# Performance work log

Hardware: AMD Instinct MI355X
Metric: run time of the kernel (lower is better)

## Reference

```python
import jax, jax.numpy as jnp
import numpy as np

BN_EPS = 1e-5


def setup_inputs() -> dict:
    key = jax.random.key(0)
    k1, k2, k3 = jax.random.split(key, 3)
    n, d = 4096, 128
    x = jax.random.normal(k1, (2 * n, d), dtype=jnp.float32)
    affinity_A = jax.random.normal(k2, (n, n), dtype=jnp.float32)
    # Xavier-uniform-like init for the [d, d] weight
    lim = float(np.sqrt(6.0 / (d + d)))
    weight = jax.random.uniform(k3, (d, d), dtype=jnp.float32, minval=-lim, maxval=lim)
    gamma = jnp.ones((d,), dtype=jnp.float32)
    beta = jnp.zeros((d,), dtype=jnp.float32)
    return {"x": x, "affinity_A": affinity_A, "weight": weight, "gamma": gamma, "beta": beta}


def reference(x, affinity_A, weight, gamma, beta):
    # Binarize affinity
    A = jnp.where(affinity_A > 0, 1.0, 0.0).astype(x.dtype)  # [n, n]
    n = A.shape[0]
    I = jnp.eye(n, dtype=x.dtype)
    # Block adjacency [[A, I], [I, A]] -> [2n, 2n]
    adj = jnp.block([[A, I], [I, A]])
    # Symmetric normalization D^{-1/2} A D^{-1/2}.
    # (Original code materializes D^{-1/2} as a full matrix and does two O(n^3)
    # matmuls; mathematically it is just row/column scaling, done here directly.)
    deg = adj.sum(axis=1)                 # [2n], >= 1 because of identity blocks
    dinv = deg ** -0.5
    norm_A = dinv[:, None] * adj * dinv[None, :]
    # GCN propagation: (norm_A @ x) @ W
    h = (norm_A @ x) @ weight             # [2n, d]
    # BatchNorm1d (training mode, biased variance) + ReLU
    mean = h.mean(axis=0)
    var = h.var(axis=0)
    h = (h - mean) * jax.lax.rsqrt(var + BN_EPS) * gamma + beta
    return jax.nn.relu(h)
```

## Files before the change

### kernel.cpp

```cpp
#include <hip/hip_runtime.h>
#include <stdint.h>


#define N_NODES 4096
#define D 128
#define TWO_N (2*N_NODES)
#define SK 8
#define KCH (N_NODES / SK)

typedef unsigned short u16;
typedef __bf16 bf16;
typedef bf16 bf16x8 __attribute__((ext_vector_type(8)));
typedef float f32x4 __attribute__((ext_vector_type(4)));
typedef u16 u16x8 __attribute__((ext_vector_type(8)));

__device__ __forceinline__ float bf2f(u16 u) {
    return __builtin_bit_cast(float, ((unsigned)u) << 16);
}
__device__ __forceinline__ u16 f2bf(float f) {
    unsigned b = __builtin_bit_cast(unsigned, f);
    unsigned r = (b + 0x7FFFu + ((b >> 16) & 1u)) >> 16;
    return (u16)r;
}
__device__ __forceinline__ bool det_fp32(const u16* gamma) {
    return gamma[0] != (u16)0x3F80;
}

__global__ void k_deg(const void* __restrict__ aff, const u16* __restrict__ gamma,
                      float* __restrict__ dinv, uint32_t* __restrict__ pack32) {
    int t = threadIdx.x;
    bool fp32 = det_fp32(gamma);
    int rl = t >> 7;
    int row = blockIdx.x * 2 + rl;
    int cl = t & 127;
    unsigned bits = 0;
    if (!fp32) {
        const u16* p = (const u16*)aff + (size_t)row * N_NODES + cl * 32;
        u16x8 v0 = *reinterpret_cast<const u16x8*>(p);
        u16x8 v1 = *reinterpret_cast<const u16x8*>(p + 8);
        u16x8 v2 = *reinterpret_cast<const u16x8*>(p + 16);
        u16x8 v3 = *reinterpret_cast<const u16x8*>(p + 24);
        #pragma unroll
        for (int e = 0; e < 8; ++e) {
            bits |= (((short)v0[e] > 0) ? 1u : 0u) << e;
            bits |= (((short)v1[e] > 0) ? 1u : 0u) << (8 + e);
            bits |= (((short)v2[e] > 0) ? 1u : 0u) << (16 + e);
            bits |= (((short)v3[e] > 0) ? 1u : 0u) << (24 + e);
        }
    } else {
        const float* p = (const float*)aff + (size_t)row * N_NODES + cl * 32;
        #pragma unroll
        for (int q = 0; q < 8; ++q) {
            f32x4 v = *reinterpret_cast<const f32x4*>(p + q * 4);
            #pragma unroll
            for (int e = 0; e < 4; ++e)
                bits |= ((v[e] > 0.f) ? 1u : 0u) << (q * 4 + e);
        }
    }
    pack32[(size_t)row * 128 + cl] = bits;
    int cnt = __popc(bits);
    #pragma unroll
    for (int off = 32; off; off >>= 1) cnt += __shfl_down(cnt, off, 64);
    __shared__ int sc[4];
    if ((t & 63) == 0) sc[t >> 6] = cnt;
    __syncthreads();
    if (t < 2)
        dinv[blockIdx.x * 2 + t] = rsqrtf((float)(sc[t * 2] + sc[t * 2 + 1] + 1));
}

__global__ void k_scale(const void* __restrict__ x, const void* __restrict__ W,
                        const u16* __restrict__ gamma, const float* __restrict__ dinv,
                        u16* __restrict__ XsT, u16* __restrict__ WT) {
    int t = threadIdx.x;
    bool fp32 = det_fp32(gamma);

    if (blockIdx.x >= 512) {
        const u16* W16 = (const u16*)W;
        const float* W32 = (const float*)W;
        int o = (blockIdx.x - 512) * 16 + (t >> 4);
        int cg = (t & 15) * 8;
        u16x8 wv;
        #pragma unroll
        for (int e = 0; e < 8; ++e) {
            size_t wi = (size_t)(cg + e) * D + o;
            float v = fp32 ? W32[wi] : bf2f(W16[wi]);
            wv[e] = f2bf(v);
        }
        *reinterpret_cast<u16x8*>(WT + (size_t)o * D + cg) = wv;
        return;
    }

    __shared__ u16 sx[16 * 136];
    int j0 = blockIdx.x * 8;
    {
        int rr = t >> 4;
        int c0 = (t & 15) * 8;
        size_t grow = (rr < 8) ? (size_t)(j0 + rr) : (size_t)(N_NODES + j0 + rr - 8);
        float dv = dinv[j0 + (rr & 7)];
        u16x8 o;
        if (!fp32) {
            u16x8 xv = *reinterpret_cast<const u16x8*>((const u16*)x + grow * D + c0);
            #pragma unroll
            for (int e = 0; e < 8; ++e) o[e] = f2bf(dv * bf2f(xv[e]));
        } else {
            f32x4 xa = *reinterpret_cast<const f32x4*>((const float*)x + grow * D + c0);
            f32x4 xb = *reinterpret_cast<const f32x4*>((const float*)x + grow * D + c0 + 4);
            #pragma unroll
            for (int e = 0; e < 4; ++e) {
                o[e] = f2bf(dv * xa[e]);
                o[4 + e] = f2bf(dv * xb[e]);
            }
        }
        *reinterpret_cast<u16x8*>(sx + rr * 136 + c0) = o;
    }
    __syncthreads();
    {
        int c = t;
        int rbase = (c < 128) ? 0 : 8;
        int cl = c & 127;
        u16x8 o;
        #pragma unroll
        for (int jl = 0; jl < 8; ++jl) o[jl] = sx[(rbase + jl) * 136 + cl];
        *reinterpret_cast<u16x8*>(XsT + (size_t)c * N_NODES + j0) = o;
    }
}

__launch_bounds__(256)
__global__ void k_gemm(const uint32_t* __restrict__ pack32, const u16* __restrict__ XsT,
                       u16* __restrict__ Ypart) {
    int t = threadIdx.x;
    int mt = blockIdx.x >> 3;
    int sk = blockIdx.x & 7;
    int r0 = mt * 64;
    int k0 = sk * KCH;
    int lane = t & 63, wid = t >> 6;
    int quad = lane >> 4, l15 = lane & 15;
    int shift = quad * 8;

    f32x4 acc[4][4];
    #pragma unroll
    for (int i = 0; i < 4; ++i)
        #pragma unroll
        for (int j = 0; j < 4; ++j) acc[i][j] = (f32x4){0.f, 0.f, 0.f, 0.f};

    const u16* bp[4];
    #pragma unroll
    for (int j = 0; j < 4; ++j)
        bp[j] = XsT + (size_t)(wid * 64 + j * 16 + l15) * N_NODES + k0 + quad * 8;
    const uint32_t* ap[4];
    #pragma unroll
    for (int i = 0; i < 4; ++i)
        ap[i] = pack32 + (size_t)(r0 + i * 16 + l15) * 128 + (k0 >> 5);

    u16x8 bc[2][4][2];
    uint2 ac[2][4];

    #pragma unroll
    for (int j = 0; j < 4; ++j)
        #pragma unroll
        for (int ks = 0; ks < 2; ++ks)
            bc[0][j][ks] = *reinterpret_cast<const u16x8*>(bp[j] + ks * 32);
    #pragma unroll
    for (int i = 0; i < 4; ++i) ac[0][i] = *reinterpret_cast<const uint2*>(ap[i]);

    #pragma unroll
    for (int it = 0; it < KCH / 64; ++it) {
        int cur = it & 1, nxt = cur ^ 1;
        if (it < KCH / 64 - 1) {
            int off = (it + 1) * 64;
            #pragma unroll
            for (int j = 0; j < 4; ++j)
                #pragma unroll
                for (int ks = 0; ks < 2; ++ks)
                    bc[nxt][j][ks] = *reinterpret_cast<const u16x8*>(bp[j] + off + ks * 32);
            #pragma unroll
            for (int i = 0; i < 4; ++i)
                ac[nxt][i] = *reinterpret_cast<const uint2*>(ap[i] + (it + 1) * 2);
        }
        #pragma unroll
        for (int ks = 0; ks < 2; ++ks) {
            bf16x8 af[4];
            #pragma unroll
            for (int i = 0; i < 4; ++i) {
                unsigned d = ks ? ac[cur][i].y : ac[cur][i].x;
                unsigned by = (d >> shift) & 0xFFu;
                u16x8 e;
                #pragma unroll
                for (int e2 = 0; e2 < 8; ++e2)
                    e[e2] = ((by >> e2) & 1u) ? (u16)0x3F80 : (u16)0;
                af[i] = __builtin_bit_cast(bf16x8, e);
            }
            #pragma unroll
            for (int i = 0; i < 4; ++i)
                #pragma unroll
                for (int j = 0; j < 4; ++j)
                    acc[i][j] = __builtin_amdgcn_mfma_f32_16x16x32_bf16(
                        af[i], __builtin_bit_cast(bf16x8, bc[cur][j][ks]), acc[i][j], 0, 0, 0);
        }
    }

    u16* yp = Ypart + (size_t)sk * N_NODES * 256;
    #pragma unroll
    for (int i = 0; i < 4; ++i) {
        int row = r0 + i * 16 + quad * 4;
        #pragma unroll
        for (int j = 0; j < 4; ++j) {
            int col = wid * 64 + j * 16 + l15;
            #pragma unroll
            for (int r = 0; r < 4; ++r)
                yp[(size_t)(row + r) * 256 + col] = f2bf(acc[i][j][r]);
        }
    }
}

__global__ void k_comb(const u16* __restrict__ Ypart, const void* __restrict__ x,
                       const u16* __restrict__ WT, const u16* __restrict__ gamma,
                       const float* __restrict__ dinv, u16* __restrict__ hpre,
                       float* __restrict__ pS, float* __restrict__ pQ) {
    __shared__ u16 sH[16 * 136];
    __shared__ u16 sWT[128 * 136];
    __shared__ float sOut[16 * 132];
    int t = threadIdx.x;
    bool fp32 = det_fp32(gamma);
    int r0 = blockIdx.x * 16;
    bool top = blockIdx.x < 256;
    int node0 = top ? r0 : r0 - N_NODES;
    const u16* x16 = (const u16*)x;
    const float* x32 = (const float*)x;

    {
        int r = t >> 4;
        int c0 = (t & 15) * 8;
        int node = node0 + r;
        int ycol = (top ? 0 : 128) + c0;
        float fs[8] = {0.f, 0.f, 0.f, 0.f, 0.f, 0.f, 0.f, 0.f};
        #pragma unroll
        for (int sk = 0; sk < SK; ++sk) {
            u16x8 yv = *reinterpret_cast<const u16x8*>(Ypart + ((size_t)sk * N_NODES + node) * 256 + ycol);
            #pragma unroll
            for (int e = 0; e < 8; ++e) fs[e] += bf2f(yv[e]);
        }
        float dv = dinv[node];
        size_t xi = (top ? (size_t)(N_NODES + node) : (size_t)node) * D + c0;
        u16x8 hv;
        if (!fp32) {
            u16x8 xv = *reinterpret_cast<const u16x8*>(x16 + xi);
            #pragma unroll
            for (int e = 0; e < 8; ++e) hv[e] = f2bf(dv * fs[e] + dv * dv * bf2f(xv[e]));
        } else {
            f32x4 xa = *reinterpret_cast<const f32x4*>(x32 + xi);
            f32x4 xb = *reinterpret_cast<const f32x4*>(x32 + xi + 4);
            #pragma unroll
            for (int e = 0; e < 4; ++e) {
                hv[e]     = f2bf(dv * fs[e]     + dv * dv * xa[e]);
                hv[4 + e] = f2bf(dv * fs[4 + e] + dv * dv * xb[e]);
            }
        }
        *reinterpret_cast<u16x8*>(sH + r * 136 + c0) = hv;
    }
    #pragma unroll
    for (int p = 0; p < 8; ++p) {
        int idx = p * 256 + t;
        int o = idx >> 4;
        int cg = (idx & 15) * 8;
        u16x8 wv = *reinterpret_cast<const u16x8*>(WT + (size_t)o * D + cg);
        *reinterpret_cast<u16x8*>(sWT + o * 136 + cg) = wv;
    }
    __syncthreads();

    int lane = t & 63, wid = t >> 6;
    int quad = lane >> 4, l15 = lane & 15;
    f32x4 acc[2];
    acc[0] = (f32x4){0.f, 0.f, 0.f, 0.f};
    acc[1] = (f32x4){0.f, 0.f, 0.f, 0.f};
    #pragma unroll
    for (int ks = 0; ks < 4; ++ks) {
        bf16x8 af = *reinterpret_cast<const bf16x8*>(sH + l15 * 136 + ks * 32 + quad * 8);
        #pragma unroll
        for (int j = 0; j < 2; ++j) {
            bf16x8 bfr = *reinterpret_cast<const bf16x8*>(sWT + (wid * 32 + j * 16 + l15) * 136 + ks * 32 + quad * 8);
            acc[j] = __builtin_amdgcn_mfma_f32_16x16x32_bf16(af, bfr, acc[j], 0, 0, 0);
        }
    }
    #pragma unroll
    for (int j = 0; j < 2; ++j) {
        int row = quad * 4;
        int col = wid * 32 + j * 16 + l15;
        #pragma unroll
        for (int r = 0; r < 4; ++r) sOut[(row + r) * 132 + col] = acc[j][r];
    }
    __syncthreads();
    #pragma unroll
    for (int p = 0; p < 8; ++p) {
        int idx = p * 256 + t;
        int r = idx >> 7, c = idx & 127;
        hpre[(size_t)(r0 + r) * D + c] = f2bf(sOut[r * 132 + c]);
    }
    if (t < 128) {
        float s = 0.f, q = 0.f;
        #pragma unroll
        for (int r = 0; r < 16; ++r) {
            float v = sOut[r * 132 + t];
            s += v; q += v * v;
        }
        pS[blockIdx.x * 128 + t] = s;
        pQ[blockIdx.x * 128 + t] = q;
    }
}

__global__ void k_stats(const float* __restrict__ pS, const float* __restrict__ pQ,
                        const void* __restrict__ gamma, const void* __restrict__ beta,
                        const u16* __restrict__ gdet, float* __restrict__ scsh) {
    __shared__ float rs[256], rq[256];
    int t = threadIdx.x;
    int c0 = blockIdx.x * 8;
    int cl = t & 7;
    int rr = t >> 3;
    float s = 0.f, q = 0.f;
    #pragma unroll
    for (int i = 0; i < 16; ++i) {
        int row = rr + i * 32;
        s += pS[row * 128 + c0 + cl];
        q += pQ[row * 128 + c0 + cl];
    }
    rs[t] = s; rq[t] = q;
    __syncthreads();
    #pragma unroll
    for (int st = 128; st >= 8; st >>= 1) {
        if (t < st) { rs[t] += rs[t + st]; rq[t] += rq[t + st]; }
        __syncthreads();
    }
    if (t < 8) {
        bool fp32 = det_fp32(gdet);
        int c = c0 + t;
        float mean = rs[t] * (1.0f / TWO_N);
        float var = fmaxf(rq[t] * (1.0f / TWO_N) - mean * mean, 0.f);
        float inv = rsqrtf(var + 1e-5f);
        float g = fp32 ? ((const float*)gamma)[c] : bf2f(((const u16*)gamma)[c]);
        float b = fp32 ? ((const float*)beta)[c]  : bf2f(((const u16*)beta)[c]);
        scsh[c] = inv * g;
        scsh[128 + c] = b - mean * inv * g;
    }
}

__global__ void k_bn(const u16* __restrict__ hpre, const float* __restrict__ scsh,
                     const u16* __restrict__ gdet, void* __restrict__ out) {
    __shared__ float ssc[128], ssh[128];
    int t = threadIdx.x;
    bool fp32 = det_fp32(gdet);
    if (t < 128) { ssc[t] = scsh[t]; ssh[t] = scsh[128 + t]; }
    __syncthreads();
    size_t base = (size_t)blockIdx.x * 2048 + t * 8;
    int c0 = (t & 15) * 8;
    u16x8 hv = *reinterpret_cast<const u16x8*>(hpre + base);
    if (!fp32) {
        u16x8 ov;
        #pragma unroll
        for (int e = 0; e < 8; ++e) {
            float v = bf2f(hv[e]) * ssc[c0 + e] + ssh[c0 + e];
            ov[e] = f2bf(fmaxf(v, 0.f));
        }
        *reinterpret_cast<u16x8*>((u16*)out + base) = ov;
    } else {
        float* o = (float*)out + base;
        #pragma unroll
        for (int e = 0; e < 8; ++e) {
            float v = bf2f(hv[e]) * ssc[c0 + e] + ssh[c0 + e];
            o[e] = fmaxf(v, 0.f);
        }
    }
}

extern "C" void kernel_launch(void* const* d_in, const int* in_sizes, int n_in,
                              void* d_out, int out_size, void* d_ws, size_t ws_size,
                              hipStream_t stream) {
    const void* x = d_in[0];
    const void* aff = d_in[1];
    const void* W = d_in[2];
    const u16* gamma = (const u16*)d_in[3];
    const void* beta = d_in[4];

    char* ws = (char*)d_ws;
    uint32_t* pack32 = (uint32_t*)ws;
    u16* XsT = (u16*)(ws + 2097152);
    u16* Ypart = (u16*)(ws + 4194304);
    u16* hpre = (u16*)(ws + 20971520);
    float* dinv = (float*)(ws + 23068672);
    u16* WT = (u16*)(ws + 23085056);
    float* pS = (float*)(ws + 23117824);
    float* pQ = (float*)(ws + 23379968);
    float* scsh = (float*)(ws + 23642112);

    k_deg<<<2048, 256, 0, stream>>>(aff, gamma, dinv, pack32);
    k_scale<<<520, 256, 0, stream>>>(x, W, gamma, dinv, XsT, WT);
    k_gemm<<<512, 256, 0, stream>>>(pack32, XsT, Ypart);
    k_comb<<<512, 256, 0, stream>>>(Ypart, x, WT, gamma, dinv, hpre, pS, pQ);
    k_stats<<<16, 256, 0, stream>>>(pS, pQ, gamma, beta, gamma, scsh);
    k_bn<<<512, 256, 0, stream>>>(hpre, scsh, gamma, d_out);
}
```

Before: 145.3 us.

## Shrink gemm row tile to 32, triple-buffer loads, widen comb tile to 32 rows

The binarized-adjacency GEMM now uses 32-row tiles instead of 64, doubling the grid to 1024 blocks with a launch-bounds occupancy hint. The K loop steps 32 at a time with a three-stage register prefetch ring. The combine kernel now processes 32 rows per block with a 2x2 warp layout, halving its grid and the partial-stat rows that k_stats must reduce. The aim is more parallelism and latency hiding in the main GEMM at the cost of re-reading the XsT operand twice as often.

```diff
diff --git a/kernel.cpp b/kernel.cpp
--- a/kernel.cpp
+++ b/kernel.cpp
@@ -125,21 +125,21 @@
     }
 }
 
-__launch_bounds__(256)
+__launch_bounds__(256, 4)
 __global__ void k_gemm(const uint32_t* __restrict__ pack32, const u16* __restrict__ XsT,
                        u16* __restrict__ Ypart) {
     int t = threadIdx.x;
     int mt = blockIdx.x >> 3;
     int sk = blockIdx.x & 7;
-    int r0 = mt * 64;
+    int r0 = mt * 32;
     int k0 = sk * KCH;
     int lane = t & 63, wid = t >> 6;
     int quad = lane >> 4, l15 = lane & 15;
     int shift = quad * 8;
 
-    f32x4 acc[4][4];
-    #pragma unroll
-    for (int i = 0; i < 4; ++i)
+    f32x4 acc[2][4];
+    #pragma unroll
+    for (int i = 0; i < 2; ++i)
         #pragma unroll
         for (int j = 0; j < 4; ++j) acc[i][j] = (f32x4){0.f, 0.f, 0.f, 0.f};
 
@@ -147,61 +147,52 @@
     #pragma unroll
     for (int j = 0; j < 4; ++j)
         bp[j] = XsT + (size_t)(wid * 64 + j * 16 + l15) * N_NODES + k0 + quad * 8;
-    const uint32_t* ap[4];
-    #pragma unroll
-    for (int i = 0; i < 4; ++i)
+    const uint32_t* ap[2];
+    #pragma unroll
+    for (int i = 0; i < 2; ++i)
         ap[i] = pack32 + (size_t)(r0 + i * 16 + l15) * 128 + (k0 >> 5);
 
-    u16x8 bc[2][4][2];
-    uint2 ac[2][4];
-
-    #pragma unroll
-    for (int j = 0; j < 4; ++j)
-        #pragma unroll
-        for (int ks = 0; ks < 2; ++ks)
-            bc[0][j][ks] = *reinterpret_cast<const u16x8*>(bp[j] + ks * 32);
-    #pragma unroll
-    for (int i = 0; i < 4; ++i) ac[0][i] = *reinterpret_cast<const uint2*>(ap[i]);
-
-    #pragma unroll
-    for (int it = 0; it < KCH / 64; ++it) {
-        int cur = it & 1, nxt = cur ^ 1;
-        if (it < KCH / 64 - 1) {
-            int off = (it + 1) * 64;
+    u16x8 bb[3][4];
+    uint32_t ab[3][2];
+    #pragma unroll
+    for (int s = 0; s < 2; ++s) {
+        #pragma unroll
+        for (int j = 0; j < 4; ++j) bb[s][j] = *reinterpret_cast<const u16x8*>(bp[j] + s * 32);
+        #pragma unroll
+        for (int i = 0; i < 2; ++i) ab[s][i] = ap[i][s];
+    }
+
+    #pragma unroll
+    for (int s = 0; s < KCH / 32; ++s) {
+        int cur = s % 3, pre = (s + 2) % 3;
+        if (s < KCH / 32 - 2) {
             #pragma unroll
             for (int j = 0; j < 4; ++j)
-                #pragma unroll
-                for (int ks = 0; ks < 2; ++ks)
-                    bc[nxt][j][ks] = *reinterpret_cast<const u16x8*>(bp[j] + off + ks * 32);
-            #pragma unroll
-            for (int i = 0; i < 4; ++i)
-                ac[nxt][i] = *reinterpret_cast<const uint2*>(ap[i] + (it + 1) * 2);
-        }
-        #pragma unroll
-        for (int ks = 0; ks < 2; ++ks) {
-            bf16x8 af[4];
-            #pragma unroll
-            for (int i = 0; i < 4; ++i) {
-                unsigned d = ks ? ac[cur][i].y : ac[cur][i].x;
-                unsigned by = (d >> shift) & 0xFFu;
-                u16x8 e;
-                #pragma unroll
-                for (int e2 = 0; e2 < 8; ++e2)
-                    e[e2] = ((by >> e2) & 1u) ? (u16)0x3F80 : (u16)0;
-                af[i] = __builtin_bit_cast(bf16x8, e);
-            }
-            #pragma unroll
-            for (int i = 0; i < 4; ++i)
-                #pragma unroll
-                for (int j = 0; j < 4; ++j)
-                    acc[i][j] = __builtin_amdgcn_mfma_f32_16x16x32_bf16(
-                        af[i], __builtin_bit_cast(bf16x8, bc[cur][j][ks]), acc[i][j], 0, 0, 0);
-        }
+                bb[pre][j] = *reinterpret_cast<const u16x8*>(bp[j] + (s + 2) * 32);
+            #pragma unroll
+            for (int i = 0; i < 2; ++i) ab[pre][i] = ap[i][s + 2];
+        }
+        bf16x8 af[2];
+        #pragma unroll
+        for (int i = 0; i < 2; ++i) {
+            unsigned by = (ab[cur][i] >> shift) & 0xFFu;
+            u16x8 e;
+            #pragma unroll
+            for (int e2 = 0; e2 < 8; ++e2)
+                e[e2] = ((by >> e2) & 1u) ? (u16)0x3F80 : (u16)0;
+            af[i] = __builtin_bit_cast(bf16x8, e);
+        }
+        #pragma unroll
+        for (int i = 0; i < 2; ++i)
+            #pragma unroll
+            for (int j = 0; j < 4; ++j)
+                acc[i][j] = __builtin_amdgcn_mfma_f32_16x16x32_bf16(
+                    af[i], __builtin_bit_cast(bf16x8, bb[cur][j]), acc[i][j], 0, 0, 0);
     }
 
     u16* yp = Ypart + (size_t)sk * N_NODES * 256;
     #pragma unroll
-    for (int i = 0; i < 4; ++i) {
+    for (int i = 0; i < 2; ++i) {
         int row = r0 + i * 16 + quad * 4;
         #pragma unroll
         for (int j = 0; j < 4; ++j) {
@@ -217,19 +208,20 @@
                        const u16* __restrict__ WT, const u16* __restrict__ gamma,
                        const float* __restrict__ dinv, u16* __restrict__ hpre,
                        float* __restrict__ pS, float* __restrict__ pQ) {
-    __shared__ u16 sH[16 * 136];
+    __shared__ u16 sH[32 * 136];
     __shared__ u16 sWT[128 * 136];
-    __shared__ float sOut[16 * 132];
+    __shared__ float sOut[32 * 132];
     int t = threadIdx.x;
     bool fp32 = det_fp32(gamma);
-    int r0 = blockIdx.x * 16;
-    bool top = blockIdx.x < 256;
+    int r0 = blockIdx.x * 32;
+    bool top = blockIdx.x < 128;
     int node0 = top ? r0 : r0 - N_NODES;
     const u16* x16 = (const u16*)x;
     const float* x32 = (const float*)x;
 
-    {
-        int r = t >> 4;
+    #pragma unroll
+    for (int p = 0; p < 2; ++p) {
+        int r = p * 16 + (t >> 4);
         int c0 = (t & 15) * 8;
         int node = node0 + r;
         int ycol = (top ? 0 : 128) + c0;
@@ -269,29 +261,30 @@
     __syncthreads();
 
     int lane = t & 63, wid = t >> 6;
+    int wm2 = wid >> 1, wn2 = wid & 1;
     int quad = lane >> 4, l15 = lane & 15;
-    f32x4 acc[2];
-    acc[0] = (f32x4){0.f, 0.f, 0.f, 0.f};
-    acc[1] = (f32x4){0.f, 0.f, 0.f, 0.f};
+    f32x4 acc2[4];
+    #pragma unroll
+    for (int j = 0; j < 4; ++j) acc2[j] = (f32x4){0.f, 0.f, 0.f, 0.f};
     #pragma unroll
     for (int ks = 0; ks < 4; ++ks) {
-        bf16x8 af = *reinterpret_cast<const bf16x8*>(sH + l15 * 136 + ks * 32 + quad * 8);
-        #pragma unroll
-        for (int j = 0; j < 2; ++j) {
-            bf16x8 bfr = *reinterpret_cast<const bf16x8*>(sWT + (wid * 32 + j * 16 + l15) * 136 + ks * 32 + quad * 8);
-            acc[j] = __builtin_amdgcn_mfma_f32_16x16x32_bf16(af, bfr, acc[j], 0, 0, 0);
-        }
-    }
-    #pragma unroll
-    for (int j = 0; j < 2; ++j) {
-        int row = quad * 4;
-        int col = wid * 32 + j * 16 + l15;
-        #pragma unroll
-        for (int r = 0; r < 4; ++r) sOut[(row + r) * 132 + col] = acc[j][r];
-    }
-    __syncthreads();
-    #pragma unroll
-    for (int p = 0; p < 8; ++p) {
+        bf16x8 af = *reinterpret_cast<const bf16x8*>(sH + (wm2 * 16 + l15) * 136 + ks * 32 + quad * 8);
+        #pragma unroll
+        for (int j = 0; j < 4; ++j) {
+            bf16x8 bfr = *reinterpret_cast<const bf16x8*>(sWT + (wn2 * 64 + j * 16 + l15) * 136 + ks * 32 + quad * 8);
+            acc2[j] = __builtin_amdgcn_mfma_f32_16x16x32_bf16(af, bfr, acc2[j], 0, 0, 0);
+        }
+    }
+    #pragma unroll
+    for (int j = 0; j < 4; ++j) {
+        int row = wm2 * 16 + quad * 4;
+        int col = wn2 * 64 + j * 16 + l15;
+        #pragma unroll
+        for (int r = 0; r < 4; ++r) sOut[(row + r) * 132 + col] = acc2[j][r];
+    }
+    __syncthreads();
+    #pragma unroll
+    for (int p = 0; p < 16; ++p) {
         int idx = p * 256 + t;
         int r = idx >> 7, c = idx & 127;
         hpre[(size_t)(r0 + r) * D + c] = f2bf(sOut[r * 132 + c]);
@@ -299,7 +292,7 @@
     if (t < 128) {
         float s = 0.f, q = 0.f;
         #pragma unroll
-        for (int r = 0; r < 16; ++r) {
+        for (int r = 0; r < 32; ++r) {
             float v = sOut[r * 132 + t];
             s += v; q += v * v;
         }
@@ -318,7 +311,7 @@
     int rr = t >> 3;
     float s = 0.f, q = 0.f;
     #pragma unroll
-    for (int i = 0; i < 16; ++i) {
+    for (int i = 0; i < 8; ++i) {
         int row = rr + i * 32;
         s += pS[row * 128 + c0 + cl];
         q += pQ[row * 128 + c0 + cl];
@@ -388,13 +381,13 @@
     float* dinv = (float*)(ws + 23068672);
     u16* WT = (u16*)(ws + 23085056);
     float* pS = (float*)(ws + 23117824);
-    float* pQ = (float*)(ws + 23379968);
-    float* scsh = (float*)(ws + 23642112);
+    float* pQ = (float*)(ws + 23248896);
+    float* scsh = (float*)(ws + 23379968);
 
     k_deg<<<2048, 256, 0, stream>>>(aff, gamma, dinv, pack32);
     k_scale<<<520, 256, 0, stream>>>(x, W, gamma, dinv, XsT, WT);
-    k_gemm<<<512, 256, 0, stream>>>(pack32, XsT, Ypart);
-    k_comb<<<512, 256, 0, stream>>>(Ypart, x, WT, gamma, dinv, hpre, pS, pQ);
+    k_gemm<<<1024, 256, 0, stream>>>(pack32, XsT, Ypart);
+    k_comb<<<256, 256, 0, stream>>>(Ypart, x, WT, gamma, dinv, hpre, pS, pQ);
     k_stats<<<16, 256, 0, stream>>>(pS, pQ, gamma, beta, gamma, scsh);
     k_bn<<<512, 256, 0, stream>>>(hpre, scsh, gamma, d_out);
 }
```

New measurement: 157.1 us. 1.08x slower.

## Halve GEMM split-K, split output columns, enlarge combine tiles, move W transpose

Applied to the files above, without the earlier changes.

The main GEMM now splits K four ways instead of eight and instead splits the 256 output columns into two halves per block. This halves the bf16 partial-sum traffic that the combine kernel has to read and reduce. The combine kernel now processes 32 rows per block with a 2x2 wave layout, which halves the number of times the W tile is staged into shared memory. The W transpose moves from k_scale into extra blocks of k_deg, and the workspace offsets shrink to match. In exchange, each GEMM block re-reads the packed A bits for both column halves, and each block runs a longer K loop with fewer accumulators.

```diff
diff --git a/kernel.cpp b/kernel.cpp
--- a/kernel.cpp
+++ b/kernel.cpp
@@ -5,7 +5,7 @@
 #define N_NODES 4096
 #define D 128
 #define TWO_N (2*N_NODES)
-#define SK 8
+#define SK 4
 #define KCH (N_NODES / SK)
 
 typedef unsigned short u16;
@@ -26,10 +26,28 @@
     return gamma[0] != (u16)0x3F80;
 }
 
-__global__ void k_deg(const void* __restrict__ aff, const u16* __restrict__ gamma,
-                      float* __restrict__ dinv, uint32_t* __restrict__ pack32) {
+__global__ void k_deg(const void* __restrict__ aff, const void* __restrict__ W,
+                      const u16* __restrict__ gamma, float* __restrict__ dinv,
+                      uint32_t* __restrict__ pack32, u16* __restrict__ WT) {
     int t = threadIdx.x;
     bool fp32 = det_fp32(gamma);
+
+    if (blockIdx.x >= 2048) {
+        const u16* W16 = (const u16*)W;
+        const float* W32 = (const float*)W;
+        int o = (blockIdx.x - 2048) * 16 + (t >> 4);
+        int cg = (t & 15) * 8;
+        u16x8 wv;
+        #pragma unroll
+        for (int e = 0; e < 8; ++e) {
+            size_t wi = (size_t)(cg + e) * D + o;
+            float v = fp32 ? W32[wi] : bf2f(W16[wi]);
+            wv[e] = f2bf(v);
+        }
+        *reinterpret_cast<u16x8*>(WT + (size_t)o * D + cg) = wv;
+        return;
+    }
+
     int rl = t >> 7;
     int row = blockIdx.x * 2 + rl;
     int cl = t & 127;
@@ -68,28 +86,10 @@
         dinv[blockIdx.x * 2 + t] = rsqrtf((float)(sc[t * 2] + sc[t * 2 + 1] + 1));
 }
 
-__global__ void k_scale(const void* __restrict__ x, const void* __restrict__ W,
-                        const u16* __restrict__ gamma, const float* __restrict__ dinv,
-                        u16* __restrict__ XsT, u16* __restrict__ WT) {
+__global__ void k_scale(const void* __restrict__ x, const u16* __restrict__ gamma,
+                        const float* __restrict__ dinv, u16* __restrict__ XsT) {
     int t = threadIdx.x;
     bool fp32 = det_fp32(gamma);
-
-    if (blockIdx.x >= 512) {
-        const u16* W16 = (const u16*)W;
-        const float* W32 = (const float*)W;
-        int o = (blockIdx.x - 512) * 16 + (t >> 4);
-        int cg = (t & 15) * 8;
-        u16x8 wv;
-        #pragma unroll
-        for (int e = 0; e < 8; ++e) {
-            size_t wi = (size_t)(cg + e) * D + o;
-            float v = fp32 ? W32[wi] : bf2f(W16[wi]);
-            wv[e] = f2bf(v);
-        }
-        *reinterpret_cast<u16x8*>(WT + (size_t)o * D + cg) = wv;
-        return;
-    }
-
     __shared__ u16 sx[16 * 136];
     int j0 = blockIdx.x * 8;
     {
@@ -130,33 +130,35 @@
                        u16* __restrict__ Ypart) {
     int t = threadIdx.x;
     int mt = blockIdx.x >> 3;
-    int sk = blockIdx.x & 7;
+    int nh = (blockIdx.x >> 2) & 1;
+    int sk = blockIdx.x & 3;
     int r0 = mt * 64;
+    int cb = nh * 128;
     int k0 = sk * KCH;
     int lane = t & 63, wid = t >> 6;
     int quad = lane >> 4, l15 = lane & 15;
     int shift = quad * 8;
 
-    f32x4 acc[4][4];
+    f32x4 acc[4][2];
     #pragma unroll
     for (int i = 0; i < 4; ++i)
         #pragma unroll
-        for (int j = 0; j < 4; ++j) acc[i][j] = (f32x4){0.f, 0.f, 0.f, 0.f};
-
-    const u16* bp[4];
-    #pragma unroll
-    for (int j = 0; j < 4; ++j)
-        bp[j] = XsT + (size_t)(wid * 64 + j * 16 + l15) * N_NODES + k0 + quad * 8;
+        for (int j = 0; j < 2; ++j) acc[i][j] = (f32x4){0.f, 0.f, 0.f, 0.f};
+
+    const u16* bp[2];
+    #pragma unroll
+    for (int j = 0; j < 2; ++j)
+        bp[j] = XsT + (size_t)(cb + wid * 32 + j * 16 + l15) * N_NODES + k0 + quad * 8;
     const uint32_t* ap[4];
     #pragma unroll
     for (int i = 0; i < 4; ++i)
         ap[i] = pack32 + (size_t)(r0 + i * 16 + l15) * 128 + (k0 >> 5);
 
-    u16x8 bc[2][4][2];
+    u16x8 bc[2][2][2];
     uint2 ac[2][4];
 
     #pragma unroll
-    for (int j = 0; j < 4; ++j)
+    for (int j = 0; j < 2; ++j)
         #pragma unroll
         for (int ks = 0; ks < 2; ++ks)
             bc[0][j][ks] = *reinterpret_cast<const u16x8*>(bp[j] + ks * 32);
@@ -169,7 +171,7 @@
         if (it < KCH / 64 - 1) {
             int off = (it + 1) * 64;
             #pragma unroll
-            for (int j = 0; j < 4; ++j)
+            for (int j = 0; j < 2; ++j)
                 #pragma unroll
                 for (int ks = 0; ks < 2; ++ks)
                     bc[nxt][j][ks] = *reinterpret_cast<const u16x8*>(bp[j] + off + ks * 32);
@@ -193,7 +195,7 @@
             #pragma unroll
             for (int i = 0; i < 4; ++i)
                 #pragma unroll
-                for (int j = 0; j < 4; ++j)
+                for (int j = 0; j < 2; ++j)
                     acc[i][j] = __builtin_amdgcn_mfma_f32_16x16x32_bf16(
                         af[i], __builtin_bit_cast(bf16x8, bc[cur][j][ks]), acc[i][j], 0, 0, 0);
         }
@@ -204,8 +206,8 @@
     for (int i = 0; i < 4; ++i) {
         int row = r0 + i * 16 + quad * 4;
         #pragma unroll
-        for (int j = 0; j < 4; ++j) {
-            int col = wid * 64 + j * 16 + l15;
+        for (int j = 0; j < 2; ++j) {
+            int col = cb + wid * 32 + j * 16 + l15;
             #pragma unroll
             for (int r = 0; r < 4; ++r)
                 yp[(size_t)(row + r) * 256 + col] = f2bf(acc[i][j][r]);
@@ -217,19 +219,20 @@
                        const u16* __restrict__ WT, const u16* __restrict__ gamma,
                        const float* __restrict__ dinv, u16* __restrict__ hpre,
                        float* __restrict__ pS, float* __restrict__ pQ) {
-    __shared__ u16 sH[16 * 136];
+    __shared__ u16 sH[32 * 136];
     __shared__ u16 sWT[128 * 136];
-    __shared__ float sOut[16 * 132];
+    __shared__ float sOut[32 * 132];
     int t = threadIdx.x;
     bool fp32 = det_fp32(gamma);
-    int r0 = blockIdx.x * 16;
-    bool top = blockIdx.x < 256;
+    int r0 = blockIdx.x * 32;
+    bool top = blockIdx.x < 128;
     int node0 = top ? r0 : r0 - N_NODES;
     const u16* x16 = (const u16*)x;
     const float* x32 = (const float*)x;
 
-    {
-        int r = t >> 4;
+    #pragma unroll
+    for (int p = 0; p < 2; ++p) {
+        int r = p * 16 + (t >> 4);
         int c0 = (t & 15) * 8;
         int node = node0 + r;
         int ycol = (top ? 0 : 128) + c0;
@@ -269,29 +272,30 @@
     __syncthreads();
 
     int lane = t & 63, wid = t >> 6;
+    int wm2 = wid >> 1, wn2 = wid & 1;
     int quad = lane >> 4, l15 = lane & 15;
-    f32x4 acc[2];
-    acc[0] = (f32x4){0.f, 0.f, 0.f, 0.f};
-    acc[1] = (f32x4){0.f, 0.f, 0.f, 0.f};
+    f32x4 acc2[4];
+    #pragma unroll
+    for (int j = 0; j < 4; ++j) acc2[j] = (f32x4){0.f, 0.f, 0.f, 0.f};
     #pragma unroll
     for (int ks = 0; ks < 4; ++ks) {
-        bf16x8 af = *reinterpret_cast<const bf16x8*>(sH + l15 * 136 + ks * 32 + quad * 8);
-        #pragma unroll
-        for (int j = 0; j < 2; ++j) {
-            bf16x8 bfr = *reinterpret_cast<const bf16x8*>(sWT + (wid * 32 + j * 16 + l15) * 136 + ks * 32 + quad * 8);
-            acc[j] = __builtin_amdgcn_mfma_f32_16x16x32_bf16(af, bfr, acc[j], 0, 0, 0);
-        }
-    }
-    #pragma unroll
-    for (int j = 0; j < 2; ++j) {
-        int row = quad * 4;
-        int col = wid * 32 + j * 16 + l15;
-        #pragma unroll
-        for (int r = 0; r < 4; ++r) sOut[(row + r) * 132 + col] = acc[j][r];
-    }
-    __syncthreads();
-    #pragma unroll
-    for (int p = 0; p < 8; ++p) {
+        bf16x8 af = *reinterpret_cast<const bf16x8*>(sH + (wm2 * 16 + l15) * 136 + ks * 32 + quad * 8);
+        #pragma unroll
+        for (int j = 0; j < 4; ++j) {
+            bf16x8 bfr = *reinterpret_cast<const bf16x8*>(sWT + (wn2 * 64 + j * 16 + l15) * 136 + ks * 32 + quad * 8);
+            acc2[j] = __builtin_amdgcn_mfma_f32_16x16x32_bf16(af, bfr, acc2[j], 0, 0, 0);
+        }
+    }
+    #pragma unroll
+    for (int j = 0; j < 4; ++j) {
+        int row = wm2 * 16 + quad * 4;
+        int col = wn2 * 64 + j * 16 + l15;
+        #pragma unroll
+        for (int r = 0; r < 4; ++r) sOut[(row + r) * 132 + col] = acc2[j][r];
+    }
+    __syncthreads();
+    #pragma unroll
+    for (int p = 0; p < 16; ++p) {
         int idx = p * 256 + t;
         int r = idx >> 7, c = idx & 127;
         hpre[(size_t)(r0 + r) * D + c] = f2bf(sOut[r * 132 + c]);
@@ -299,7 +303,7 @@
     if (t < 128) {
         float s = 0.f, q = 0.f;
         #pragma unroll
-        for (int r = 0; r < 16; ++r) {
+        for (int r = 0; r < 32; ++r) {
             float v = sOut[r * 132 + t];
             s += v; q += v * v;
         }
@@ -318,7 +322,7 @@
     int rr = t >> 3;
     float s = 0.f, q = 0.f;
     #pragma unroll
-    for (int i = 0; i < 16; ++i) {
+    for (int i = 0; i < 8; ++i) {
         int row = rr + i * 32;
         s += pS[row * 128 + c0 + cl];
         q += pQ[row * 128 + c0 + cl];
@@ -384,17 +388,17 @@
     uint32_t* pack32 = (uint32_t*)ws;
     u16* XsT = (u16*)(ws + 2097152);
     u16* Ypart = (u16*)(ws + 4194304);
-    u16* hpre = (u16*)(ws + 20971520);
-    float* dinv = (float*)(ws + 23068672);
-    u16* WT = (u16*)(ws + 23085056);
-    float* pS = (float*)(ws + 23117824);
-    float* pQ = (float*)(ws + 23379968);
-    float* scsh = (float*)(ws + 23642112);
-
-    k_deg<<<2048, 256, 0, stream>>>(aff, gamma, dinv, pack32);
-    k_scale<<<520, 256, 0, stream>>>(x, W, gamma, dinv, XsT, WT);
+    u16* hpre = (u16*)(ws + 12582912);
+    float* dinv = (float*)(ws + 14680064);
+    u16* WT = (u16*)(ws + 14696448);
+    float* pS = (float*)(ws + 14729216);
+    float* pQ = (float*)(ws + 14860288);
+    float* scsh = (float*)(ws + 14991360);
+
+    k_deg<<<2056, 256, 0, stream>>>(aff, W, gamma, dinv, pack32, WT);
+    k_scale<<<512, 256, 0, stream>>>(x, gamma, dinv, XsT);
     k_gemm<<<512, 256, 0, stream>>>(pack32, XsT, Ypart);
-    k_comb<<<512, 256, 0, stream>>>(Ypart, x, WT, gamma, dinv, hpre, pS, pQ);
+    k_comb<<<256, 256, 0, stream>>>(Ypart, x, WT, gamma, dinv, hpre, pS, pQ);
     k_stats<<<16, 256, 0, stream>>>(pS, pQ, gamma, beta, gamma, scsh);
     k_bn<<<512, 256, 0, stream>>>(hpre, scsh, gamma, d_out);
 }
```

Measured after the change: 143.7 us. No clear change (-1.1%).
